# Kernel optimization log

Measured on AMD Instinct MI355X. Metric: run time of the kernel, lower is better.

## Reference

```python
import jax, jax.numpy as jnp
import numpy as np

IN_F, OUT_F = 4096, 16384
B, S = 4, 2048
SCALE = 0.02

def setup_inputs() -> dict:
    key = jax.random.key(0)
    k1, k2 = jax.random.split(key)
    x = jax.random.normal(k1, (B, S, IN_F), dtype=jnp.float32)
    # ternary weights in {-1, 0, +1}
    weight_ternary = jax.random.randint(k2, (OUT_F, IN_F), -1, 2, dtype=jnp.int32)
    weight_scale = jnp.full((1,), SCALE, dtype=jnp.float32)
    return {"x": x, "weight_ternary": weight_ternary, "weight_scale": weight_scale}

def reference(x, weight_ternary, weight_scale):
    # dequantize ternary weight
    w = weight_ternary.astype(jnp.float32) * weight_scale  # [OUT_F, IN_F]
    # per-token int8 activation quant/dequant
    x_scale = jnp.clip(jnp.max(jnp.abs(x), axis=-1, keepdims=True), 1e-5, None)
    x_quant = jnp.round(jnp.clip(x / x_scale * 127.0, -128.0, 127.0))
    x_final = x_quant * x_scale / 127.0
    # linear: x_final @ w.T
    return jnp.einsum('bsi,oi->bso', x_final, w)
```

## Files before the change

kernel.cpp:

```cpp
#include <hip/hip_runtime.h>

#define IN_F 4096
#define OUT_F 16384
#define MTOK 8192

#define BM 256
#define BN 256
#define BKB 128
#define NKT (IN_F / BKB)
#define NIT (NKT / 2)

typedef __attribute__((ext_vector_type(4))) int   i32x4;
typedef __attribute__((ext_vector_type(4))) float f32x4;

__device__ __forceinline__ void gload_lds16(const void* g, void* l) {
    __builtin_amdgcn_global_load_lds(
        (const __attribute__((address_space(1))) void*)g,
        (__attribute__((address_space(3))) void*)l,
        16, 0, 0);
}

__global__ __launch_bounds__(256) void k_quant(const float* __restrict__ x,
                                               char* __restrict__ xq,
                                               float* __restrict__ xs) {
    const int m = blockIdx.x;
    const int t = threadIdx.x;
    const float* xrow = x + (size_t)m * IN_F;

    f32x4 v[4];
    float mx = 0.f;
#pragma unroll
    for (int i = 0; i < 4; ++i) {
        v[i] = *(const f32x4*)&xrow[(i * 256 + t) * 4];
        mx = fmaxf(mx, fmaxf(fmaxf(fabsf(v[i].x), fabsf(v[i].y)),
                             fmaxf(fabsf(v[i].z), fabsf(v[i].w))));
    }
#pragma unroll
    for (int off = 32; off > 0; off >>= 1)
        mx = fmaxf(mx, __shfl_xor(mx, off));

    __shared__ float wmax[4];
    const int wid = t >> 6;
    if ((t & 63) == 0) wmax[wid] = mx;
    __syncthreads();
    const float scale = fmaxf(fmaxf(fmaxf(wmax[0], wmax[1]),
                                    fmaxf(wmax[2], wmax[3])), 1e-5f);
    const float inv = 127.0f / scale;

    int* xqi = (int*)(xq + (size_t)m * IN_F);
#pragma unroll
    for (int i = 0; i < 4; ++i) {
        int q0 = (int)rintf(fminf(fmaxf(v[i].x * inv, -128.f), 127.f));
        int q1 = (int)rintf(fminf(fmaxf(v[i].y * inv, -128.f), 127.f));
        int q2 = (int)rintf(fminf(fmaxf(v[i].z * inv, -128.f), 127.f));
        int q3 = (int)rintf(fminf(fmaxf(v[i].w * inv, -128.f), 127.f));
        xqi[i * 256 + t] = (q0 & 255) | ((q1 & 255) << 8) |
                           ((q2 & 255) << 16) | (q3 << 24);
    }
    if (t == 0) xs[m] = scale;
}

__global__ __launch_bounds__(256) void k_wconv(const int* __restrict__ wt,
                                               int* __restrict__ w8) {
    const int total4 = OUT_F * IN_F / 4;
    int idx = blockIdx.x * 256 + threadIdx.x;
    const int stride = gridDim.x * 256;
    for (; idx < total4; idx += stride) {
        i32x4 w = *(const i32x4*)&wt[(size_t)idx * 4];
        w8[idx] = (w.x & 255) | ((w.y & 255) << 8) |
                  ((w.z & 255) << 16) | (w.w << 24);
    }
}

__global__ __launch_bounds__(512, 2) void k_gemm(
    const char*  __restrict__ Aq,
    const char*  __restrict__ Bq,
    const float* __restrict__ xs,
    const float* __restrict__ wsp,
    float*       __restrict__ C) {
    __shared__ __align__(16) char lds[131072];

    const int t    = threadIdx.x;
    const int lane = t & 63;
    const int wid  = t >> 6;
    const int wr   = wid >> 2;
    const int wc   = wid & 3;

    const int bid = blockIdx.x;
    const int bn  = (bid & 7) * 8 + ((bid >> 3) & 7);
    const int bm  = bid >> 6;
    const int mBase = bm * BM;
    const int nBase = bn * BN;

    const int r0 = t >> 3;
    const int c0 = ((t ^ r0) & 7) * 16;

#define STAGE_A(h, b, kt) do {                                                 \
        const size_t _s = (size_t)(mBase + (h) * 128 + r0) * IN_F + c0         \
                        + (size_t)(kt) * BKB;                                  \
        char* _d = lds + (b) * 32768 + (h) * 16384 + wid * 1024;               \
        gload_lds16(Aq + _s, _d);                                              \
        gload_lds16(Aq + _s + (size_t)64 * IN_F, _d + 8192);                   \
    } while (0)
#define STAGE_B(h, b, kt) do {                                                 \
        const size_t _s = (size_t)(nBase + (h) * 128 + r0) * IN_F + c0         \
                        + (size_t)(kt) * BKB;                                  \
        char* _d = lds + 65536 + (b) * 32768 + (h) * 16384 + wid * 1024;       \
        gload_lds16(Bq + _s, _d);                                              \
        gload_lds16(Bq + _s + (size_t)64 * IN_F, _d + 8192);                   \
    } while (0)

    const int slot  = (((lane >> 4) ^ (lane & 7)) << 4);
    const int aOff0 = (lane & 15) * 128 + slot;
    const int bOff0 = ((wc & 1) * 64 + (lane & 15)) * 128 + slot;
    const char* ldsA = lds + wr * 16384;
    const char* ldsB = lds + 65536 + (wc >> 1) * 16384;

#define RD_A(dst, bOfs, miB)                                                   \
    _Pragma("unroll")                                                          \
    for (int mi = 0; mi < 4; ++mi) {                                           \
        dst[mi][0] = *(const i32x4*)(ldsA + (bOfs) + ((miB) + mi) * 2048 + aOff0);        \
        dst[mi][1] = *(const i32x4*)(ldsA + (bOfs) + ((miB) + mi) * 2048 + (aOff0 ^ 64)); \
    }
#define RD_B(dst, bOfs, niB)                                                   \
    _Pragma("unroll")                                                          \
    for (int ni = 0; ni < 2; ++ni) {                                           \
        dst[ni][0] = *(const i32x4*)(ldsB + (bOfs) + ((niB) + ni) * 2048 + bOff0);        \
        dst[ni][1] = *(const i32x4*)(ldsB + (bOfs) + ((niB) + ni) * 2048 + (bOff0 ^ 64)); \
    }
#define MFMA_Q(A, MIB, B, NIB)                                                 \
    __builtin_amdgcn_s_setprio(1);                                             \
    _Pragma("unroll")                                                          \
    for (int mi = 0; mi < 4; ++mi)                                             \
        _Pragma("unroll")                                                      \
        for (int ni = 0; ni < 2; ++ni)                                         \
            _Pragma("unroll")                                                  \
            for (int kk = 0; kk < 2; ++kk)                                     \
                acc[(MIB) + mi][(NIB) + ni] =                                  \
                    __builtin_amdgcn_mfma_i32_16x16x64_i8(                     \
                        A[mi][kk], B[ni][kk], acc[(MIB) + mi][(NIB) + ni],     \
                        0, 0, 0);                                              \
    __builtin_amdgcn_s_setprio(0);
#define BAR()   __builtin_amdgcn_s_barrier()
#define LGKM0() asm volatile("s_waitcnt lgkmcnt(0)" ::: "memory")
#define VM6()   asm volatile("s_waitcnt vmcnt(6)" ::: "memory")
#define VM0()   asm volatile("s_waitcnt vmcnt(0)" ::: "memory")

    i32x4 acc[8][4];
#pragma unroll
    for (int i = 0; i < 8; ++i)
#pragma unroll
        for (int j = 0; j < 4; ++j)
            acc[i][j] = (i32x4){0, 0, 0, 0};

    i32x4 aLo[4][2], aHi[4][2], bLo[2][2], bHi[2][2];

    STAGE_A(0, 0, 0); STAGE_A(1, 0, 0); STAGE_B(0, 0, 0); STAGE_B(1, 0, 0);
    STAGE_B(0, 1, 1); STAGE_B(1, 1, 1); STAGE_A(0, 1, 1);
    VM6();
    BAR();

    for (int it = 0; it < NIT; ++it) {
        const int kt1 = 2 * it + 1;
        const int kn0 = 2 * it + 2;
        const int kn1 = 2 * it + 3;
        const bool more = (it < NIT - 1);

        RD_A(aLo, 0, 0); RD_B(bLo, 0, 0);
        STAGE_A(1, 1, kt1);
        BAR(); LGKM0();
        MFMA_Q(aLo, 0, bLo, 0);
        BAR();
        RD_B(bHi, 0, 2);
        if (more) STAGE_B(0, 0, kn0);
        BAR(); LGKM0();
        MFMA_Q(aLo, 0, bHi, 2);
        BAR();
        RD_A(aHi, 0, 4);
        if (more) STAGE_B(1, 0, kn0);
        BAR(); LGKM0();
        MFMA_Q(aHi, 4, bHi, 2);
        BAR();
        if (more) STAGE_A(0, 0, kn0);
        BAR();
        MFMA_Q(aHi, 4, bLo, 0);
        if (more) { VM6(); } else { VM0(); }
        BAR();
        RD_A(aLo, 32768, 0); RD_B(bLo, 32768, 0);
        if (more) STAGE_A(1, 0, kn0);
        BAR(); LGKM0();
        MFMA_Q(aLo, 0, bLo, 0);
        BAR();
        RD_B(bHi, 32768, 2);
        if (more) STAGE_B(0, 1, kn1);
        BAR(); LGKM0();
        MFMA_Q(aLo, 0, bHi, 2);
        BAR();
        RD_A(aHi, 32768, 4);
        if (more) STAGE_B(1, 1, kn1);
        BAR(); LGKM0();
        MFMA_Q(aHi, 4, bHi, 2);
        BAR();
        if (more) STAGE_A(0, 1, kn1);
        BAR();
        MFMA_Q(aHi, 4, bLo, 0);
        if (more) { VM6(); } else { VM0(); }
        BAR();
    }

    const float wsc = wsp[0] * (1.0f / 127.0f);
#pragma unroll
    for (int mi = 0; mi < 8; ++mi) {
        float rs[4];
#pragma unroll
        for (int r = 0; r < 4; ++r)
            rs[r] = xs[mBase + wr * 128 + mi * 16 + (lane >> 4) * 4 + r] * wsc;
#pragma unroll
        for (int ni = 0; ni < 4; ++ni) {
            const int col = nBase + wc * 64 + ni * 16 + (lane & 15);
#pragma unroll
            for (int r = 0; r < 4; ++r) {
                const int row = mBase + wr * 128 + mi * 16 + (lane >> 4) * 4 + r;
                C[(size_t)row * OUT_F + col] = (float)acc[mi][ni][r] * rs[r];
            }
        }
    }
}

extern "C" void kernel_launch(void* const* d_in, const int* in_sizes, int n_in,
                              void* d_out, int out_size, void* d_ws, size_t ws_size,
                              hipStream_t stream) {
    const float* x   = (const float*)d_in[0];
    const int*   wt  = (const int*)d_in[1];
    const float* wsp = (const float*)d_in[2];
    float* out = (float*)d_out;

    char*  w8 = (char*)d_ws;
    char*  xq = (char*)d_ws + (size_t)OUT_F * IN_F;
    float* xs = (float*)((char*)d_ws + (size_t)OUT_F * IN_F
                                     + (size_t)MTOK * IN_F);

    k_wconv<<<8192, 256, 0, stream>>>(wt, (int*)w8);
    k_quant<<<MTOK, 256, 0, stream>>>(x, xq, xs);

    const int grid = (MTOK / BM) * (OUT_F / BN);
    k_gemm<<<grid, 512, 0, stream>>>(xq, w8, xs, wsp, out);
}
```

Measured before the change: 577.6 us.

## Switch int8 GEMM main loop to 32x32x32 MFMA tiles

Replaces the 16x16x64 int8 MFMA with the 32x32x32 variant. LDS fragment reads, swizzle offsets, accumulator layout, loop phases and epilogue indexing are reorganised to match. The larger MFMA tile is meant to cut LDS reads per MFMA and raise operand reuse, easing LDS bandwidth pressure. It also changes the interleaving of global-to-LDS staging with compute, which risks different latency hiding.

```diff
diff --git a/kernel.cpp b/kernel.cpp
--- a/kernel.cpp
+++ b/kernel.cpp
@@ -10,8 +10,9 @@
 #define NKT (IN_F / BKB)
 #define NIT (NKT / 2)
 
-typedef __attribute__((ext_vector_type(4))) int   i32x4;
-typedef __attribute__((ext_vector_type(4))) float f32x4;
+typedef __attribute__((ext_vector_type(4)))  int   i32x4;
+typedef __attribute__((ext_vector_type(16))) int   i32x16;
+typedef __attribute__((ext_vector_type(4)))  float f32x4;
 
 __device__ __forceinline__ void gload_lds16(const void* g, void* l) {
     __builtin_amdgcn_global_load_lds(
@@ -110,50 +111,51 @@
         gload_lds16(Bq + _s + (size_t)64 * IN_F, _d + 8192);                   \
     } while (0)
 
-    const int slot  = (((lane >> 4) ^ (lane & 7)) << 4);
-    const int aOff0 = (lane & 15) * 128 + slot;
-    const int bOff0 = ((wc & 1) * 64 + (lane & 15)) * 128 + slot;
+    const int h  = lane >> 5;
+    const int r7 = lane & 7;
+    int aOffKs[4], bOffKs[4];
+#pragma unroll
+    for (int ks = 0; ks < 4; ++ks) {
+        const int slot = (((2 * ks + h) ^ r7) << 4);
+        aOffKs[ks] = (lane & 31) * 128 + slot;
+        bOffKs[ks] = ((wc & 1) * 64 + (lane & 31)) * 128 + slot;
+    }
     const char* ldsA = lds + wr * 16384;
     const char* ldsB = lds + 65536 + (wc >> 1) * 16384;
 
-#define RD_A(dst, bOfs, miB)                                                   \
+#define RD_A2(dst, bOfs, miB)                                                  \
     _Pragma("unroll")                                                          \
-    for (int mi = 0; mi < 4; ++mi) {                                           \
-        dst[mi][0] = *(const i32x4*)(ldsA + (bOfs) + ((miB) + mi) * 2048 + aOff0);        \
-        dst[mi][1] = *(const i32x4*)(ldsA + (bOfs) + ((miB) + mi) * 2048 + (aOff0 ^ 64)); \
-    }
-#define RD_B(dst, bOfs, niB)                                                   \
+    for (int mi = 0; mi < 2; ++mi)                                             \
+        _Pragma("unroll")                                                      \
+        for (int ks = 0; ks < 4; ++ks)                                         \
+            dst[mi][ks] = *(const i32x4*)(ldsA + (bOfs) +                      \
+                              ((miB) + mi) * 4096 + aOffKs[ks]);
+#define RD_B1(dst, bOfs, ni)                                                   \
     _Pragma("unroll")                                                          \
-    for (int ni = 0; ni < 2; ++ni) {                                           \
-        dst[ni][0] = *(const i32x4*)(ldsB + (bOfs) + ((niB) + ni) * 2048 + bOff0);        \
-        dst[ni][1] = *(const i32x4*)(ldsB + (bOfs) + ((niB) + ni) * 2048 + (bOff0 ^ 64)); \
-    }
-#define MFMA_Q(A, MIB, B, NIB)                                                 \
+    for (int ks = 0; ks < 4; ++ks)                                             \
+        dst[ks] = *(const i32x4*)(ldsB + (bOfs) + (ni) * 4096 + bOffKs[ks]);
+#define MFMA_Q(Af, MIB, Bf, NI)                                                \
     __builtin_amdgcn_s_setprio(1);                                             \
     _Pragma("unroll")                                                          \
-    for (int mi = 0; mi < 4; ++mi)                                             \
+    for (int ks = 0; ks < 4; ++ks)                                             \
         _Pragma("unroll")                                                      \
-        for (int ni = 0; ni < 2; ++ni)                                         \
-            _Pragma("unroll")                                                  \
-            for (int kk = 0; kk < 2; ++kk)                                     \
-                acc[(MIB) + mi][(NIB) + ni] =                                  \
-                    __builtin_amdgcn_mfma_i32_16x16x64_i8(                     \
-                        A[mi][kk], B[ni][kk], acc[(MIB) + mi][(NIB) + ni],     \
-                        0, 0, 0);                                              \
+        for (int mi = 0; mi < 2; ++mi)                                         \
+            acc[(MIB) + mi][NI] = __builtin_amdgcn_mfma_i32_32x32x32_i8(       \
+                Af[mi][ks], Bf[ks], acc[(MIB) + mi][NI], 0, 0, 0);             \
     __builtin_amdgcn_s_setprio(0);
 #define BAR()   __builtin_amdgcn_s_barrier()
 #define LGKM0() asm volatile("s_waitcnt lgkmcnt(0)" ::: "memory")
 #define VM6()   asm volatile("s_waitcnt vmcnt(6)" ::: "memory")
 #define VM0()   asm volatile("s_waitcnt vmcnt(0)" ::: "memory")
 
-    i32x4 acc[8][4];
-#pragma unroll
-    for (int i = 0; i < 8; ++i)
-#pragma unroll
-        for (int j = 0; j < 4; ++j)
-            acc[i][j] = (i32x4){0, 0, 0, 0};
-
-    i32x4 aLo[4][2], aHi[4][2], bLo[2][2], bHi[2][2];
+    i32x16 acc[4][2];
+#pragma unroll
+    for (int i = 0; i < 4; ++i)
+#pragma unroll
+        for (int j = 0; j < 2; ++j)
+            acc[i][j] = (i32x16)(0);
+
+    i32x4 aLo[2][4], aHi[2][4], b0[4], b1[4];
 
     STAGE_A(0, 0, 0); STAGE_A(1, 0, 0); STAGE_B(0, 0, 0); STAGE_B(1, 0, 0);
     STAGE_B(0, 1, 1); STAGE_B(1, 1, 1); STAGE_A(0, 1, 1);
@@ -166,62 +168,60 @@
         const int kn1 = 2 * it + 3;
         const bool more = (it < NIT - 1);
 
-        RD_A(aLo, 0, 0); RD_B(bLo, 0, 0);
+        RD_A2(aLo, 0, 0); RD_B1(b0, 0, 0);
         STAGE_A(1, 1, kt1);
         BAR(); LGKM0();
-        MFMA_Q(aLo, 0, bLo, 0);
-        BAR();
-        RD_B(bHi, 0, 2);
+        MFMA_Q(aLo, 0, b0, 0);
+        BAR();
+        RD_B1(b1, 0, 1);
+        BAR(); LGKM0();
+        MFMA_Q(aLo, 0, b1, 1);
+        BAR();
+        RD_A2(aHi, 0, 2);
         if (more) STAGE_B(0, 0, kn0);
         BAR(); LGKM0();
-        MFMA_Q(aLo, 0, bHi, 2);
-        BAR();
-        RD_A(aHi, 0, 4);
-        if (more) STAGE_B(1, 0, kn0);
-        BAR(); LGKM0();
-        MFMA_Q(aHi, 4, bHi, 2);
-        BAR();
-        if (more) STAGE_A(0, 0, kn0);
-        BAR();
-        MFMA_Q(aHi, 4, bLo, 0);
+        MFMA_Q(aHi, 2, b1, 1);
+        BAR();
+        if (more) { STAGE_B(1, 0, kn0); STAGE_A(0, 0, kn0); }
+        BAR();
+        MFMA_Q(aHi, 2, b0, 0);
         if (more) { VM6(); } else { VM0(); }
         BAR();
-        RD_A(aLo, 32768, 0); RD_B(bLo, 32768, 0);
+        RD_A2(aLo, 32768, 0); RD_B1(b0, 32768, 0);
         if (more) STAGE_A(1, 0, kn0);
         BAR(); LGKM0();
-        MFMA_Q(aLo, 0, bLo, 0);
-        BAR();
-        RD_B(bHi, 32768, 2);
+        MFMA_Q(aLo, 0, b0, 0);
+        BAR();
+        RD_B1(b1, 32768, 1);
+        BAR(); LGKM0();
+        MFMA_Q(aLo, 0, b1, 1);
+        BAR();
+        RD_A2(aHi, 32768, 2);
         if (more) STAGE_B(0, 1, kn1);
         BAR(); LGKM0();
-        MFMA_Q(aLo, 0, bHi, 2);
-        BAR();
-        RD_A(aHi, 32768, 4);
-        if (more) STAGE_B(1, 1, kn1);
-        BAR(); LGKM0();
-        MFMA_Q(aHi, 4, bHi, 2);
-        BAR();
-        if (more) STAGE_A(0, 1, kn1);
-        BAR();
-        MFMA_Q(aHi, 4, bLo, 0);
+        MFMA_Q(aHi, 2, b1, 1);
+        BAR();
+        if (more) { STAGE_B(1, 1, kn1); STAGE_A(0, 1, kn1); }
+        BAR();
+        MFMA_Q(aHi, 2, b0, 0);
         if (more) { VM6(); } else { VM0(); }
         BAR();
     }
 
     const float wsc = wsp[0] * (1.0f / 127.0f);
 #pragma unroll
-    for (int mi = 0; mi < 8; ++mi) {
-        float rs[4];
-#pragma unroll
-        for (int r = 0; r < 4; ++r)
-            rs[r] = xs[mBase + wr * 128 + mi * 16 + (lane >> 4) * 4 + r] * wsc;
-#pragma unroll
-        for (int ni = 0; ni < 4; ++ni) {
-            const int col = nBase + wc * 64 + ni * 16 + (lane & 15);
-#pragma unroll
-            for (int r = 0; r < 4; ++r) {
-                const int row = mBase + wr * 128 + mi * 16 + (lane >> 4) * 4 + r;
-                C[(size_t)row * OUT_F + col] = (float)acc[mi][ni][r] * rs[r];
+    for (int mi = 0; mi < 4; ++mi) {
+#pragma unroll
+        for (int rq = 0; rq < 4; ++rq) {
+            const int rowB = mBase + wr * 128 + mi * 32 + rq * 8 + h * 4;
+            const f32x4 s4 = *(const f32x4*)&xs[rowB];
+#pragma unroll
+            for (int ni = 0; ni < 2; ++ni) {
+                const int col = nBase + wc * 64 + ni * 32 + (lane & 31);
+#pragma unroll
+                for (int r = 0; r < 4; ++r)
+                    C[(size_t)(rowB + r) * OUT_F + col] =
+                        (float)acc[mi][ni][rq * 4 + r] * (s4[r] * wsc);
             }
         }
     }
```

Result: slower. 640.7 us (+10.9%).

## Use 16 waves per GEMM block with 64x64 per-wave tiles

Applied to the files above, without the earlier changes.

The int8 GEMM block goes from 512 to 1024 threads. Each of the 16 waves now owns a 64x64 output subtile instead of 128x64, so each thread issues one 16-byte global-to-LDS load per stage instead of two, and the vmcnt waits are adjusted to match. The LDS read offsets and fragment arrays are reshaped to fit. This halves accumulator registers per wave and doubles wave count for more latency hiding, at the cost of more LDS reads per MFMA and more barrier overhead. The __launch_bounds__(1024,4) hint asks for more resident waves than 128KB of LDS per block may allow.

```diff
diff --git a/kernel.cpp b/kernel.cpp
--- a/kernel.cpp
+++ b/kernel.cpp
@@ -10,8 +10,8 @@
 #define NKT (IN_F / BKB)
 #define NIT (NKT / 2)
 
-typedef __attribute__((ext_vector_type(4))) int   i32x4;
-typedef __attribute__((ext_vector_type(4))) float f32x4;
+typedef __attribute__((ext_vector_type(4)))  int   i32x4;
+typedef __attribute__((ext_vector_type(4)))  float f32x4;
 
 __device__ __forceinline__ void gload_lds16(const void* g, void* l) {
     __builtin_amdgcn_global_load_lds(
@@ -72,7 +72,7 @@
     }
 }
 
-__global__ __launch_bounds__(512, 2) void k_gemm(
+__global__ __launch_bounds__(1024, 4) void k_gemm(
     const char*  __restrict__ Aq,
     const char*  __restrict__ Bq,
     const float* __restrict__ xs,
@@ -84,7 +84,7 @@
     const int lane = t & 63;
     const int wid  = t >> 6;
     const int wr   = wid >> 2;
-    const int wc   = wid & 3;
+    const int wcn  = wid & 3;
 
     const int bid = blockIdx.x;
     const int bn  = (bid & 7) * 8 + ((bid >> 3) & 7);
@@ -93,71 +93,68 @@
     const int nBase = bn * BN;
 
     const int r0 = t >> 3;
-    const int c0 = ((t ^ r0) & 7) * 16;
-
-#define STAGE_A(h, b, kt) do {                                                 \
-        const size_t _s = (size_t)(mBase + (h) * 128 + r0) * IN_F + c0         \
-                        + (size_t)(kt) * BKB;                                  \
-        char* _d = lds + (b) * 32768 + (h) * 16384 + wid * 1024;               \
-        gload_lds16(Aq + _s, _d);                                              \
-        gload_lds16(Aq + _s + (size_t)64 * IN_F, _d + 8192);                   \
-    } while (0)
-#define STAGE_B(h, b, kt) do {                                                 \
-        const size_t _s = (size_t)(nBase + (h) * 128 + r0) * IN_F + c0         \
-                        + (size_t)(kt) * BKB;                                  \
-        char* _d = lds + 65536 + (b) * 32768 + (h) * 16384 + wid * 1024;       \
-        gload_lds16(Bq + _s, _d);                                              \
-        gload_lds16(Bq + _s + (size_t)64 * IN_F, _d + 8192);                   \
-    } while (0)
-
-    const int slot  = (((lane >> 4) ^ (lane & 7)) << 4);
-    const int aOff0 = (lane & 15) * 128 + slot;
-    const int bOff0 = ((wc & 1) * 64 + (lane & 15)) * 128 + slot;
-    const char* ldsA = lds + wr * 16384;
-    const char* ldsB = lds + 65536 + (wc >> 1) * 16384;
+    const int c0 = ((t ^ (t >> 3)) & 7) << 4;
+
+#define STAGE_A(h, b, kt)                                                      \
+    gload_lds16(Aq + (size_t)(mBase + (h) * 128 + r0) * IN_F + c0              \
+                   + (size_t)(kt) * BKB,                                       \
+                lds + (b) * 32768 + (h) * 16384 + wid * 1024)
+#define STAGE_B(h, b, kt)                                                      \
+    gload_lds16(Bq + (size_t)(nBase + (h) * 128 + r0) * IN_F + c0              \
+                   + (size_t)(kt) * BKB,                                       \
+                lds + 65536 + (b) * 32768 + (h) * 16384 + wid * 1024)
+
+    int aOff[2];
+#pragma unroll
+    for (int kk = 0; kk < 2; ++kk)
+        aOff[kk] = (lane & 15) * 128 + (((kk * 4 + (lane >> 4)) ^ (lane & 7)) << 4);
+    const char* ldsA = lds + wr * 8192;
+    const char* ldsB = lds + 65536 + wcn * 8192;
 
 #define RD_A(dst, bOfs, miB)                                                   \
     _Pragma("unroll")                                                          \
-    for (int mi = 0; mi < 4; ++mi) {                                           \
-        dst[mi][0] = *(const i32x4*)(ldsA + (bOfs) + ((miB) + mi) * 2048 + aOff0);        \
-        dst[mi][1] = *(const i32x4*)(ldsA + (bOfs) + ((miB) + mi) * 2048 + (aOff0 ^ 64)); \
-    }
+    for (int mi = 0; mi < 2; ++mi)                                             \
+        _Pragma("unroll")                                                      \
+        for (int kk = 0; kk < 2; ++kk)                                         \
+            dst[mi][kk] = *(const i32x4*)(ldsA + (bOfs) +                      \
+                              ((miB) + mi) * 2048 + aOff[kk]);
 #define RD_B(dst, bOfs, niB)                                                   \
     _Pragma("unroll")                                                          \
-    for (int ni = 0; ni < 2; ++ni) {                                           \
-        dst[ni][0] = *(const i32x4*)(ldsB + (bOfs) + ((niB) + ni) * 2048 + bOff0);        \
-        dst[ni][1] = *(const i32x4*)(ldsB + (bOfs) + ((niB) + ni) * 2048 + (bOff0 ^ 64)); \
-    }
-#define MFMA_Q(A, MIB, B, NIB)                                                 \
+    for (int ni = 0; ni < 2; ++ni)                                             \
+        _Pragma("unroll")                                                      \
+        for (int kk = 0; kk < 2; ++kk)                                         \
+            dst[ni][kk] = *(const i32x4*)(ldsB + (bOfs) +                      \
+                              ((niB) + ni) * 2048 + aOff[kk]);
+#define MFMA_Q(Af, MIB, Bf, NIB)                                               \
     __builtin_amdgcn_s_setprio(1);                                             \
     _Pragma("unroll")                                                          \
-    for (int mi = 0; mi < 4; ++mi)                                             \
+    for (int kk = 0; kk < 2; ++kk)                                             \
         _Pragma("unroll")                                                      \
-        for (int ni = 0; ni < 2; ++ni)                                         \
+        for (int mi = 0; mi < 2; ++mi)                                         \
             _Pragma("unroll")                                                  \
-            for (int kk = 0; kk < 2; ++kk)                                     \
+            for (int ni = 0; ni < 2; ++ni)                                     \
                 acc[(MIB) + mi][(NIB) + ni] =                                  \
                     __builtin_amdgcn_mfma_i32_16x16x64_i8(                     \
-                        A[mi][kk], B[ni][kk], acc[(MIB) + mi][(NIB) + ni],     \
+                        Af[mi][kk], Bf[ni][kk], acc[(MIB) + mi][(NIB) + ni],   \
                         0, 0, 0);                                              \
     __builtin_amdgcn_s_setprio(0);
 #define BAR()   __builtin_amdgcn_s_barrier()
 #define LGKM0() asm volatile("s_waitcnt lgkmcnt(0)" ::: "memory")
-#define VM6()   asm volatile("s_waitcnt vmcnt(6)" ::: "memory")
+#define VM3()   asm volatile("s_waitcnt vmcnt(3)" ::: "memory")
 #define VM0()   asm volatile("s_waitcnt vmcnt(0)" ::: "memory")
 
-    i32x4 acc[8][4];
-#pragma unroll
-    for (int i = 0; i < 8; ++i)
+    i32x4 acc[4][4];
+#pragma unroll
+    for (int i = 0; i < 4; ++i)
 #pragma unroll
         for (int j = 0; j < 4; ++j)
             acc[i][j] = (i32x4){0, 0, 0, 0};
 
-    i32x4 aLo[4][2], aHi[4][2], bLo[2][2], bHi[2][2];
+    i32x4 aLo[2][2], aHi[2][2], bLo[2][2], bHi[2][2];
 
     STAGE_A(0, 0, 0); STAGE_A(1, 0, 0); STAGE_B(0, 0, 0); STAGE_B(1, 0, 0);
     STAGE_B(0, 1, 1); STAGE_B(1, 1, 1); STAGE_A(0, 1, 1);
-    VM6();
+    VM3();
     BAR();
 
     for (int it = 0; it < NIT; ++it) {
@@ -172,19 +169,18 @@
         MFMA_Q(aLo, 0, bLo, 0);
         BAR();
         RD_B(bHi, 0, 2);
-        if (more) STAGE_B(0, 0, kn0);
         BAR(); LGKM0();
         MFMA_Q(aLo, 0, bHi, 2);
         BAR();
-        RD_A(aHi, 0, 4);
-        if (more) STAGE_B(1, 0, kn0);
-        BAR(); LGKM0();
-        MFMA_Q(aHi, 4, bHi, 2);
+        RD_A(aHi, 0, 2);
+        if (more) { STAGE_B(0, 0, kn0); STAGE_B(1, 0, kn0); }
+        BAR(); LGKM0();
+        MFMA_Q(aHi, 2, bHi, 2);
         BAR();
         if (more) STAGE_A(0, 0, kn0);
         BAR();
-        MFMA_Q(aHi, 4, bLo, 0);
-        if (more) { VM6(); } else { VM0(); }
+        MFMA_Q(aHi, 2, bLo, 0);
+        if (more) { VM3(); } else { VM0(); }
         BAR();
         RD_A(aLo, 32768, 0); RD_B(bLo, 32768, 0);
         if (more) STAGE_A(1, 0, kn0);
@@ -192,35 +188,34 @@
         MFMA_Q(aLo, 0, bLo, 0);
         BAR();
         RD_B(bHi, 32768, 2);
-        if (more) STAGE_B(0, 1, kn1);
         BAR(); LGKM0();
         MFMA_Q(aLo, 0, bHi, 2);
         BAR();
-        RD_A(aHi, 32768, 4);
-        if (more) STAGE_B(1, 1, kn1);
-        BAR(); LGKM0();
-        MFMA_Q(aHi, 4, bHi, 2);
+        RD_A(aHi, 32768, 2);
+        if (more) { STAGE_B(0, 1, kn1); STAGE_B(1, 1, kn1); }
+        BAR(); LGKM0();
+        MFMA_Q(aHi, 2, bHi, 2);
         BAR();
         if (more) STAGE_A(0, 1, kn1);
         BAR();
-        MFMA_Q(aHi, 4, bLo, 0);
-        if (more) { VM6(); } else { VM0(); }
+        MFMA_Q(aHi, 2, bLo, 0);
+        if (more) { VM3(); } else { VM0(); }
         BAR();
     }
 
     const float wsc = wsp[0] * (1.0f / 127.0f);
 #pragma unroll
-    for (int mi = 0; mi < 8; ++mi) {
+    for (int mi = 0; mi < 4; ++mi) {
         float rs[4];
 #pragma unroll
         for (int r = 0; r < 4; ++r)
-            rs[r] = xs[mBase + wr * 128 + mi * 16 + (lane >> 4) * 4 + r] * wsc;
+            rs[r] = xs[mBase + wr * 64 + mi * 16 + (lane >> 4) * 4 + r] * wsc;
 #pragma unroll
         for (int ni = 0; ni < 4; ++ni) {
-            const int col = nBase + wc * 64 + ni * 16 + (lane & 15);
+            const int col = nBase + wcn * 64 + ni * 16 + (lane & 15);
 #pragma unroll
             for (int r = 0; r < 4; ++r) {
-                const int row = mBase + wr * 128 + mi * 16 + (lane >> 4) * 4 + r;
+                const int row = mBase + wr * 64 + mi * 16 + (lane >> 4) * 4 + r;
                 C[(size_t)row * OUT_F + col] = (float)acc[mi][ni][r] * rs[r];
             }
         }
@@ -244,5 +239,5 @@
     k_quant<<<MTOK, 256, 0, stream>>>(x, xq, xs);
 
     const int grid = (MTOK / BM) * (OUT_F / BN);
-    k_gemm<<<grid, 512, 0, stream>>>(xq, w8, xs, wsp, out);
-}
+    k_gemm<<<grid, 1024, 0, stream>>>(xq, w8, xs, wsp, out);
+}
```

Result: slower. 653.2 us (+13.1%).
